# Kernel optimization log

Measured on AMD Instinct MI355X. Metric: run time of the kernel, lower is better.

The kernel has to match this reference:

```python
import jax, jax.numpy as jnp
import numpy as np

B, T, S, H, A = 512, 2048, 16, 128, 4
EPS = 1e-8


def setup_inputs() -> dict:
    key = jax.random.key(0)
    ks = jax.random.split(key, 8)
    sc = lambda fan_in: 1.0 / np.sqrt(fan_in)
    return {
        "state": jax.random.normal(ks[0], (B, T, S), dtype=jnp.float32),
        "Wc1": jax.random.normal(ks[1], (S, H), dtype=jnp.float32) * sc(S),
        "bc1": jnp.zeros((H,), jnp.float32),
        "Wc2": jax.random.normal(ks[2], (H, A), dtype=jnp.float32) * sc(H),
        "bc2": jnp.zeros((A,), jnp.float32),
        "Wh1": jax.random.normal(ks[3], (S, H), dtype=jnp.float32) * sc(S),
        "bh1": jnp.zeros((H,), jnp.float32),
        "wh2": jax.random.normal(ks[4], (H,), dtype=jnp.float32) * sc(H),
        "bh2": jnp.zeros((1,), jnp.float32),
        "Wf": jax.random.normal(ks[5], (S, S), dtype=jnp.float32) * sc(S),
        "bf": jnp.zeros((S,), jnp.float32),
        "Wg": jax.random.normal(ks[6], (S, S * A), dtype=jnp.float32) * sc(S),
        "bg": jnp.zeros((S * A,), jnp.float32),
    }


def reference(state, Wc1, bc1, Wc2, bc2, Wh1, bh1, wh2, bh2, Wf, bf, Wg, bg):
    # reference controller: 2-layer MLP -> u_ref = -2 * controller(state)  [B,T,A]
    u_ref = -2.0 * (jnp.tanh(state @ Wc1 + bc1) @ Wc2 + bc2)

    # CBF h(state): MLP -> scalar per (B,T)
    def cbf(s):
        return jnp.tanh(s @ Wh1 + bh1) @ wh2 + bh2[0]  # [B,T]

    h = cbf(state)
    # delta_h = d h / d state  [B,T,S]  (torch autograd.grad on summed h)
    delta_h = jax.grad(lambda s: cbf(s).sum())(state)

    # control-affine dynamics: f [B,T,S], g [B,T,S,A]
    f = state @ Wf + bf
    g = (state @ Wg + bg).reshape(B, T, S, A)

    # CBF-QP constraint:  left . u <= right
    left = -jnp.einsum('bts,btsa->bta', delta_h, g)          # [B,T,A]
    right = h + jnp.einsum('bts,bts->bt', delta_h, f)        # [B,T]

    # QP: min 1/2 u^T I u + u_ref^T u  s.t. left.u <= right
    # Closed-form KKT solution (single inequality, identity Hessian):
    u_unc = -u_ref                                            # [B,T,A]
    viol = jnp.einsum('bta,bta->bt', left, u_unc) - right     # [B,T]
    lam = jax.nn.relu(viol) / (jnp.sum(left * left, axis=-1) + EPS)
    u = u_unc - lam[..., None] * left                         # [B,T,A]
    return u
```

## Files before the change

kernel.cpp:

```cpp
#include <hip/hip_runtime.h>
#include <hip/hip_bf16.h>

#define HDIM 128
#define SDIM 16
#define ADIM 4
#define NTOK (512 * 2048)
#define NTILE (NTOK / 16)
#define NBLK 2048
#define WPB 4
#define TPW (NTILE / (NBLK * WPB))

typedef _Float16 half4 __attribute__((ext_vector_type(4)));
typedef float f32x4 __attribute__((ext_vector_type(4)));

__device__ __forceinline__ f32x4 mm(half4 a, half4 b, f32x4 c) {
    return __builtin_amdgcn_mfma_f32_16x16x16f16(a, b, c, 0, 0, 0);
}
__device__ __forceinline__ float fast_tanh(float x) {
    float e = __expf(2.0f * x);
    return 1.0f - 2.0f * __builtin_amdgcn_rcpf(e + 1.0f);
}
__device__ __forceinline__ f32x4 tanh4(f32x4 z) {
    f32x4 r;
    r.x = fast_tanh(z.x); r.y = fast_tanh(z.y);
    r.z = fast_tanh(z.z); r.w = fast_tanh(z.w);
    return r;
}
__device__ __forceinline__ half4 toh(f32x4 v) {
    half4 h;
    h.x = (_Float16)v.x; h.y = (_Float16)v.y;
    h.z = (_Float16)v.z; h.w = (_Float16)v.w;
    return h;
}
__device__ __forceinline__ void split4(f32x4 v, half4& hi, half4& lo) {
    hi = toh(v);
    f32x4 r;
    r.x = v.x - (float)hi.x; r.y = v.y - (float)hi.y;
    r.z = v.z - (float)hi.z; r.w = v.w - (float)hi.w;
    lo = toh(r);
}
__device__ __forceinline__ float dot4(f32x4 a, f32x4 b) {
    return a.x*b.x + a.y*b.y + a.z*b.z + a.w*b.w;
}
__device__ __forceinline__ float redq(float v) {
    v += __shfl_xor(v, 16, 64);
    v += __shfl_xor(v, 32, 64);
    return v;
}

__global__ __launch_bounds__(256, 4) void cbf_qp_kernel(
    const float* __restrict__ state,
    const float* __restrict__ Wc1, const float* __restrict__ bc1,
    const float* __restrict__ Wc2, const float* __restrict__ bc2,
    const float* __restrict__ Wh1, const float* __restrict__ bh1,
    const float* __restrict__ wh2, const float* __restrict__ bh2,
    const float* __restrict__ Wf,  const float* __restrict__ bf,
    const float* __restrict__ Wg,  const float* __restrict__ bg,
    float* __restrict__ out)
{
    __shared__ __align__(16) half4 az1_s[8 * 64];
    __shared__ __align__(16) half4 aua_s[8 * 64];
    __shared__ __align__(16) half4 az2h_s[8 * 64];
    __shared__ __align__(16) half4 az2l_s[8 * 64];
    __shared__ __align__(16) half4 adhh_s[8 * 64];
    __shared__ __align__(16) half4 adhl_s[8 * 64];
    __shared__ __align__(16) half4 afh_s[64];
    __shared__ __align__(16) half4 afl_s[64];
    __shared__ __align__(16) half4 agh_s[4 * 64];
    __shared__ __align__(16) half4 agl_s[4 * 64];
    __shared__ __align__(16) float bgt_s[64];
    __shared__ __align__(16) float bc1_s[HDIM];
    __shared__ __align__(16) float bh1_s[HDIM];
    __shared__ __align__(16) float wh2_s[HDIM];

    const int tid = threadIdx.x;

    for (int idx = tid; idx < 8 * 64; idx += 256) {
        const int c = idx >> 6, lane = idx & 63;
        const int m = lane & 15, q = lane >> 4;
        half4 hz1, hua, h2h, h2l, hdh, hdl;
        #pragma unroll
        for (int e = 0; e < 4; ++e) {
            const int k = q * 4 + e;
            const int j = c * 16 + k;
            hz1[e] = (_Float16)Wc1[k * HDIM + c*16 + m];
            hua[e] = (m < ADIM) ? (_Float16)Wc2[j * ADIM + m] : (_Float16)0.f;
            float w2 = Wh1[k * HDIM + c*16 + m];
            _Float16 hh = (_Float16)w2;
            h2h[e] = hh; h2l[e] = (_Float16)(w2 - (float)hh);
            float wd = Wh1[m * HDIM + j] * wh2[j];
            _Float16 hd = (_Float16)wd;
            hdh[e] = hd; hdl[e] = (_Float16)(wd - (float)hd);
        }
        az1_s[idx] = hz1;  aua_s[idx] = hua;
        az2h_s[idx] = h2h; az2l_s[idx] = h2l;
        adhh_s[idx] = hdh; adhl_s[idx] = hdl;
    }
    if (tid < 64) {
        const int m = tid & 15, q = tid >> 4;
        half4 fh, fl;
        #pragma unroll
        for (int e = 0; e < 4; ++e) {
            float w = Wf[(q*4+e) * SDIM + m];
            _Float16 h = (_Float16)w;
            fh[e] = h; fl[e] = (_Float16)(w - (float)h);
        }
        afh_s[tid] = fh; afl_s[tid] = fl;
    }
    {
        const int a = tid >> 6, lane = tid & 63;
        const int m = lane & 15, q = lane >> 4;
        half4 gh, gl;
        #pragma unroll
        for (int e = 0; e < 4; ++e) {
            float w = Wg[(q*4+e) * 64 + m*4 + a];
            _Float16 h = (_Float16)w;
            gh[e] = h; gl[e] = (_Float16)(w - (float)h);
        }
        agh_s[tid] = gh; agl_s[tid] = gl;
    }
    if (tid < 64)
        bgt_s[(tid >> 4) * 16 + (tid & 15)] = bg[(tid & 15) * 4 + (tid >> 4)];
    if (tid < HDIM) {
        bc1_s[tid] = bc1[tid];
        bh1_s[tid] = bh1[tid];
        wh2_s[tid] = wh2[tid];
    }
    __syncthreads();

    const int lane = tid & 63;
    const int q = lane >> 4, n = lane & 15;
    const int wid = blockIdx.x * WPB + (tid >> 6);

    f32x4 bfC = *(const f32x4*)(bf + q*4);
    f32x4 uaC;
    {
        f32x4 b2 = *(const f32x4*)(bc2);
        uaC.x = q == 0 ? b2.x : 0.f; uaC.y = q == 0 ? b2.y : 0.f;
        uaC.z = q == 0 ? b2.z : 0.f; uaC.w = q == 0 ? b2.w : 0.f;
    }
    f32x4 bgC0 = *(const f32x4*)(&bgt_s[0*16 + q*4]);
    f32x4 bgC1 = *(const f32x4*)(&bgt_s[1*16 + q*4]);
    f32x4 bgC2 = *(const f32x4*)(&bgt_s[2*16 + q*4]);
    f32x4 bgC3 = *(const f32x4*)(&bgt_s[3*16 + q*4]);
    const float bh2v = bh2[0];

    for (int it = 0; it < TPW; ++it) {
        const int tile = wid * TPW + it;
        f32x4 sv = *(const f32x4*)(state + (size_t)(tile*16 + n) * SDIM + q*4);
        half4 bsh, bsl;
        split4(sv, bsh, bsl);

        f32x4 uaA = uaC, uaB = {0.f, 0.f, 0.f, 0.f};
        f32x4 dhA = {0.f, 0.f, 0.f, 0.f};
        f32x4 dhB = {0.f, 0.f, 0.f, 0.f};
        f32x4 dhC = {0.f, 0.f, 0.f, 0.f};
        float hp0 = 0.f, hp1 = 0.f;
        #pragma unroll 2
        for (int c = 0; c < 8; ++c) {
            f32x4 b1 = *(const f32x4*)(&bc1_s[c*16 + q*4]);
            f32x4 z1 = mm(az1_s[c*64 + lane], bsh, b1);
            half4 t1h = toh(tanh4(z1));
            if (c & 1) uaB = mm(aua_s[c*64 + lane], t1h, uaB);
            else       uaA = mm(aua_s[c*64 + lane], t1h, uaA);

            f32x4 b2v = *(const f32x4*)(&bh1_s[c*16 + q*4]);
            half4 a2h = az2h_s[c*64 + lane];
            f32x4 z2 = mm(a2h, bsl, b2v);
            z2 = mm(az2l_s[c*64 + lane], bsh, z2);
            z2 = mm(a2h, bsh, z2);
            f32x4 t2 = tanh4(z2);
            f32x4 s2;
            s2.x = 1.f - t2.x*t2.x; s2.y = 1.f - t2.y*t2.y;
            s2.z = 1.f - t2.z*t2.z; s2.w = 1.f - t2.w*t2.w;
            half4 s2h, s2l;
            split4(s2, s2h, s2l);
            half4 adh_h = adhh_s[c*64 + lane];
            dhA = mm(adh_h, s2h, dhA);
            dhB = mm(adhl_s[c*64 + lane], s2h, dhB);
            dhC = mm(adh_h, s2l, dhC);

            f32x4 wv = *(const f32x4*)(&wh2_s[c*16 + q*4]);
            if (c & 1) hp1 += dot4(wv, t2);
            else       hp0 += dot4(wv, t2);
        }
        f32x4 ua = uaA + uaB;
        f32x4 dh = dhA + dhB + dhC;
        float hp = hp0 + hp1;

        half4 fh = afh_s[lane], fl = afl_s[lane];
        f32x4 fD = mm(fh, bsl, bfC);
        fD = mm(fl, bsh, fD);
        fD = mm(fh, bsh, fD);
        f32x4 G0, G1, G2, G3;
        {
            half4 gh = agh_s[0*64 + lane], gl = agl_s[0*64 + lane];
            G0 = mm(gh, bsl, bgC0); G0 = mm(gl, bsh, G0); G0 = mm(gh, bsh, G0);
        }
        {
            half4 gh = agh_s[1*64 + lane], gl = agl_s[1*64 + lane];
            G1 = mm(gh, bsl, bgC1); G1 = mm(gl, bsh, G1); G1 = mm(gh, bsh, G1);
        }
        {
            half4 gh = agh_s[2*64 + lane], gl = agl_s[2*64 + lane];
            G2 = mm(gh, bsl, bgC2); G2 = mm(gl, bsh, G2); G2 = mm(gh, bsh, G2);
        }
        {
            half4 gh = agh_s[3*64 + lane], gl = agl_s[3*64 + lane];
            G3 = mm(gh, bsl, bgC3); G3 = mm(gl, bsh, G3); G3 = mm(gh, bsh, G3);
        }

        float right = redq(hp + dot4(dh, fD)) + bh2v;
        float l0 = -redq(dot4(dh, G0));
        float l1 = -redq(dot4(dh, G1));
        float l2 = -redq(dot4(dh, G2));
        float l3 = -redq(dot4(dh, G3));
        float u0 = 2.f * redq(ua.x);
        float u1 = 2.f * redq(ua.y);
        float u2 = 2.f * redq(ua.z);
        float u3 = 2.f * redq(ua.w);

        float viol = l0*u0 + l1*u1 + l2*u2 + l3*u3 - right;
        float lsq  = l0*l0 + l1*l1 + l2*l2 + l3*l3;
        float lam  = viol > 0.f ? viol / (lsq + 1e-8f) : 0.f;

        if (q == 0) {
            f32x4 uo;
            uo.x = u0 - lam*l0; uo.y = u1 - lam*l1;
            uo.z = u2 - lam*l2; uo.w = u3 - lam*l3;
            *(f32x4*)(out + (size_t)(tile*16 + n) * ADIM) = uo;
        }
    }
}

extern "C" void kernel_launch(void* const* d_in, const int* in_sizes, int n_in,
                              void* d_out, int out_size, void* d_ws, size_t ws_size,
                              hipStream_t stream) {
    (void)in_sizes; (void)n_in; (void)d_ws; (void)ws_size; (void)out_size;
    const float* state = (const float*)d_in[0];
    const float* Wc1   = (const float*)d_in[1];
    const float* bc1   = (const float*)d_in[2];
    const float* Wc2   = (const float*)d_in[3];
    const float* bc2   = (const float*)d_in[4];
    const float* Wh1   = (const float*)d_in[5];
    const float* bh1   = (const float*)d_in[6];
    const float* wh2   = (const float*)d_in[7];
    const float* bh2   = (const float*)d_in[8];
    const float* Wf    = (const float*)d_in[9];
    const float* bf    = (const float*)d_in[10];
    const float* Wg    = (const float*)d_in[11];
    const float* bg    = (const float*)d_in[12];
    float* out = (float*)d_out;

    hipLaunchKernelGGL(cbf_qp_kernel, dim3(NBLK), dim3(256), 0, stream,
                       state, Wc1, bc1, Wc2, bc2, Wh1, bh1, wh2, bh2,
                       Wf, bf, Wg, bg, out);
}
```

Baseline: 223.4 us.

## Share reciprocal in tanh, use RTZ pack converts, raise occupancy, grid-stride tiles

Computes four tanh values with a single reciprocal by multiplying the denominators together, and uses packed round-toward-zero f16 conversions in the hi/lo split. Folds the factor of 2 on u_ref into the Wc2 weights and the bias, and drops the cross-quad reduction of ua, since only quad 0 holds nonzero rows. Computes each G column and its dot product in turn so fewer accumulators stay live, raises the occupancy target from 4 to 5 blocks, and switches to a grid-stride tile loop over 2560 blocks. The shared reciprocal can overflow or lose accuracy when the denominators get large, and RTZ conversion changes rounding of the hi/lo split.

After: 230.6 us. 3.2% more time.

```diff
diff --git a/kernel.cpp b/kernel.cpp
--- a/kernel.cpp
+++ b/kernel.cpp
@@ -6,9 +6,9 @@
 #define ADIM 4
 #define NTOK (512 * 2048)
 #define NTILE (NTOK / 16)
-#define NBLK 2048
+#define NBLK 2560
 #define WPB 4
-#define TPW (NTILE / (NBLK * WPB))
+#define NW (NBLK * WPB)
 
 typedef _Float16 half4 __attribute__((ext_vector_type(4)));
 typedef float f32x4 __attribute__((ext_vector_type(4)));
@@ -16,14 +16,20 @@
 __device__ __forceinline__ f32x4 mm(half4 a, half4 b, f32x4 c) {
     return __builtin_amdgcn_mfma_f32_16x16x16f16(a, b, c, 0, 0, 0);
 }
-__device__ __forceinline__ float fast_tanh(float x) {
-    float e = __expf(2.0f * x);
-    return 1.0f - 2.0f * __builtin_amdgcn_rcpf(e + 1.0f);
-}
 __device__ __forceinline__ f32x4 tanh4(f32x4 z) {
+    const float c = 2.88539008177792681f;
+    float d0 = __builtin_amdgcn_exp2f(z.x * c) + 1.0f;
+    float d1 = __builtin_amdgcn_exp2f(z.y * c) + 1.0f;
+    float d2 = __builtin_amdgcn_exp2f(z.z * c) + 1.0f;
+    float d3 = __builtin_amdgcn_exp2f(z.w * c) + 1.0f;
+    float p01 = d0 * d1, p23 = d2 * d3;
+    float R = __builtin_amdgcn_rcpf(p01 * p23);
+    float R01 = R * p23, R23 = R * p01;
     f32x4 r;
-    r.x = fast_tanh(z.x); r.y = fast_tanh(z.y);
-    r.z = fast_tanh(z.z); r.w = fast_tanh(z.w);
+    r.x = 1.0f - 2.0f * (R01 * d1);
+    r.y = 1.0f - 2.0f * (R01 * d0);
+    r.z = 1.0f - 2.0f * (R23 * d3);
+    r.w = 1.0f - 2.0f * (R23 * d2);
     return r;
 }
 __device__ __forceinline__ half4 toh(f32x4 v) {
@@ -32,12 +38,20 @@
     h.z = (_Float16)v.z; h.w = (_Float16)v.w;
     return h;
 }
+__device__ __forceinline__ half4 toh_rtz(f32x4 v) {
+    auto a = __builtin_amdgcn_cvt_pkrtz(v.x, v.y);
+    auto b = __builtin_amdgcn_cvt_pkrtz(v.z, v.w);
+    half4 h;
+    h.x = (_Float16)a.x; h.y = (_Float16)a.y;
+    h.z = (_Float16)b.x; h.w = (_Float16)b.y;
+    return h;
+}
 __device__ __forceinline__ void split4(f32x4 v, half4& hi, half4& lo) {
-    hi = toh(v);
+    hi = toh_rtz(v);
     f32x4 r;
     r.x = v.x - (float)hi.x; r.y = v.y - (float)hi.y;
     r.z = v.z - (float)hi.z; r.w = v.w - (float)hi.w;
-    lo = toh(r);
+    lo = toh_rtz(r);
 }
 __device__ __forceinline__ float dot4(f32x4 a, f32x4 b) {
     return a.x*b.x + a.y*b.y + a.z*b.z + a.w*b.w;
@@ -48,7 +62,7 @@
     return v;
 }
 
-__global__ __launch_bounds__(256, 4) void cbf_qp_kernel(
+__global__ __launch_bounds__(256, 5) void cbf_qp_kernel(
     const float* __restrict__ state,
     const float* __restrict__ Wc1, const float* __restrict__ bc1,
     const float* __restrict__ Wc2, const float* __restrict__ bc2,
@@ -84,7 +98,8 @@
             const int k = q * 4 + e;
             const int j = c * 16 + k;
             hz1[e] = (_Float16)Wc1[k * HDIM + c*16 + m];
-            hua[e] = (m < ADIM) ? (_Float16)Wc2[j * ADIM + m] : (_Float16)0.f;
+            hua[e] = (m < ADIM) ? (_Float16)(2.0f * Wc2[j * ADIM + m])
+                                : (_Float16)0.f;
             float w2 = Wh1[k * HDIM + c*16 + m];
             _Float16 hh = (_Float16)w2;
             h2h[e] = hh; h2l[e] = (_Float16)(w2 - (float)hh);
@@ -136,17 +151,12 @@
     f32x4 uaC;
     {
         f32x4 b2 = *(const f32x4*)(bc2);
-        uaC.x = q == 0 ? b2.x : 0.f; uaC.y = q == 0 ? b2.y : 0.f;
-        uaC.z = q == 0 ? b2.z : 0.f; uaC.w = q == 0 ? b2.w : 0.f;
-    }
-    f32x4 bgC0 = *(const f32x4*)(&bgt_s[0*16 + q*4]);
-    f32x4 bgC1 = *(const f32x4*)(&bgt_s[1*16 + q*4]);
-    f32x4 bgC2 = *(const f32x4*)(&bgt_s[2*16 + q*4]);
-    f32x4 bgC3 = *(const f32x4*)(&bgt_s[3*16 + q*4]);
+        uaC.x = q == 0 ? 2.0f*b2.x : 0.f; uaC.y = q == 0 ? 2.0f*b2.y : 0.f;
+        uaC.z = q == 0 ? 2.0f*b2.z : 0.f; uaC.w = q == 0 ? 2.0f*b2.w : 0.f;
+    }
     const float bh2v = bh2[0];
 
-    for (int it = 0; it < TPW; ++it) {
-        const int tile = wid * TPW + it;
+    for (int tile = wid; tile < NTILE; tile += NW) {
         f32x4 sv = *(const f32x4*)(state + (size_t)(tile*16 + n) * SDIM + q*4);
         half4 bsh, bsl;
         split4(sv, bsh, bsl);
@@ -192,33 +202,36 @@
         f32x4 fD = mm(fh, bsl, bfC);
         fD = mm(fl, bsh, fD);
         fD = mm(fh, bsh, fD);
-        f32x4 G0, G1, G2, G3;
+
+        float right = redq(hp + dot4(dh, fD)) + bh2v;
+
+        float l0, l1, l2, l3;
         {
             half4 gh = agh_s[0*64 + lane], gl = agl_s[0*64 + lane];
-            G0 = mm(gh, bsl, bgC0); G0 = mm(gl, bsh, G0); G0 = mm(gh, bsh, G0);
+            f32x4 bgC = *(const f32x4*)(&bgt_s[0*16 + q*4]);
+            f32x4 G = mm(gh, bsl, bgC); G = mm(gl, bsh, G); G = mm(gh, bsh, G);
+            l0 = -redq(dot4(dh, G));
         }
         {
             half4 gh = agh_s[1*64 + lane], gl = agl_s[1*64 + lane];
-            G1 = mm(gh, bsl, bgC1); G1 = mm(gl, bsh, G1); G1 = mm(gh, bsh, G1);
+            f32x4 bgC = *(const f32x4*)(&bgt_s[1*16 + q*4]);
+            f32x4 G = mm(gh, bsl, bgC); G = mm(gl, bsh, G); G = mm(gh, bsh, G);
+            l1 = -redq(dot4(dh, G));
         }
         {
             half4 gh = agh_s[2*64 + lane], gl = agl_s[2*64 + lane];
-            G2 = mm(gh, bsl, bgC2); G2 = mm(gl, bsh, G2); G2 = mm(gh, bsh, G2);
+            f32x4 bgC = *(const f32x4*)(&bgt_s[2*16 + q*4]);
+            f32x4 G = mm(gh, bsl, bgC); G = mm(gl, bsh, G); G = mm(gh, bsh, G);
+            l2 = -redq(dot4(dh, G));
         }
         {
             half4 gh = agh_s[3*64 + lane], gl = agl_s[3*64 + lane];
-            G3 = mm(gh, bsl, bgC3); G3 = mm(gl, bsh, G3); G3 = mm(gh, bsh, G3);
-        }
-
-        float right = redq(hp + dot4(dh, fD)) + bh2v;
-        float l0 = -redq(dot4(dh, G0));
-        float l1 = -redq(dot4(dh, G1));
-        float l2 = -redq(dot4(dh, G2));
-        float l3 = -redq(dot4(dh, G3));
-        float u0 = 2.f * redq(ua.x);
-        float u1 = 2.f * redq(ua.y);
-        float u2 = 2.f * redq(ua.z);
-        float u3 = 2.f * redq(ua.w);
+            f32x4 bgC = *(const f32x4*)(&bgt_s[3*16 + q*4]);
+            f32x4 G = mm(gh, bsl, bgC); G = mm(gl, bsh, G); G = mm(gh, bsh, G);
+            l3 = -redq(dot4(dh, G));
+        }
+
+        float u0 = ua.x, u1 = ua.y, u2 = ua.z, u3 = ua.w;
 
         float viol = l0*u0 + l1*u1 + l2*u2 + l3*u3 - right;
         float lsq  = l0*l0 + l1*l1 + l2*l2 + l3*l3;
```
